# Optimization experiments

Hardware: AMD Instinct MI355X
Metric: run time of the kernel (lower is better)

## Reference

```python
import jax, jax.numpy as jnp
import numpy as np

DIM, DIM_HEAD, S, R = 1024, 64, 8, 2
SCALE = DIM_HEAD ** -0.5
NEG = -jnp.finfo(jnp.float32).max


def setup_inputs() -> dict:
    key = jax.random.key(0)
    ks = jax.random.split(key, 7)
    b, n = 2, 2048
    x = jax.random.normal(ks[0], (b, n, DIM), dtype=jnp.float32)
    mask = jnp.ones((b, n), dtype=bool)
    sd, rd = DIM_HEAD * S, DIM_HEAD * R
    init = lambda k, i, o: jax.random.normal(k, (i, o), dtype=jnp.float32) / np.sqrt(i)
    return {
        'x': x,
        'mask': mask,
        'Wsq': init(ks[1], DIM, sd),
        'Wsk': init(ks[2], DIM, sd),
        'Wrv': init(ks[3], DIM, rd),
        'Wrq': init(ks[4], DIM, sd),
        'Wrk': init(ks[5], DIM_HEAD, DIM_HEAD),
        'Wout': init(ks[6], sd, DIM),
    }


def _split_heads(t, h):
    # b n (h d) -> b h n d
    b, n, hd = t.shape
    return t.reshape(b, n, h, hd // h).transpose(0, 2, 1, 3)


def reference(x, mask, Wsq, Wsk, Wrv, Wrq, Wrk, Wout):
    # --- search stage ---
    sq = _split_heads(x @ Wsq, S) * SCALE          # b s i d
    sk = _split_heads(x @ Wsk, S)                  # b s j d
    search_sim = jnp.einsum('bsid,bsjd->bsij', sq, sk)
    search_sim = jnp.where(mask[:, None, None, :], search_sim, NEG)
    search_attn = jax.nn.softmax(search_sim, axis=-1)
    # --- retrieval stage ---
    rv = _split_heads(x @ Wrv, R)                  # b r j d
    retrieved = jnp.einsum('bsij,brjd->bsrid', search_attn, rv)  # b s r n d
    rq = _split_heads(x @ Wrq, S) * SCALE          # b s n d
    rk = retrieved @ Wrk                           # b s r n d
    retrieval_sim = jnp.einsum('bsnd,bsrnd->bsnr', rq, rk)
    retrieval_attn = jax.nn.softmax(retrieval_sim, axis=-1)
    out = jnp.einsum('bsnr,bsrnd->bsnd', retrieval_attn, retrieved)
    b, _, n, d = out.shape
    out = out.transpose(0, 2, 1, 3).reshape(b, n, S * d)  # b n (s d)
    return out @ Wout
```

## Files before the change

kernel.cpp:

```cpp
#include <hip/hip_runtime.h>

typedef unsigned short u16;
typedef unsigned int u32;
typedef __attribute__((ext_vector_type(8))) short short8;
typedef __attribute__((ext_vector_type(4))) float f32x4;
typedef __attribute__((ext_vector_type(16))) float f32x16;

#define B_     2
#define N_     2048
#define DIMX   1024
#define DH     64
#define NS     8
#define SD     512
#define RD     128

__device__ __forceinline__ float bu2f(u16 u) {
    return __uint_as_float(((unsigned)u) << 16);
}
__device__ __forceinline__ u16 f2bu(float f) {
    unsigned u = __float_as_uint(f);
    return (u16)((u + 0x7FFFu + ((u >> 16) & 1u)) >> 16);
}
__device__ __forceinline__ int swzA(int row, int col) {
    return row * 64 + (col ^ ((row & 7) << 3));
}
__device__ __forceinline__ int qswz(int row, int quad) {
    return row * 64 + ((quad ^ (row & 15)) << 2);
}
__device__ __forceinline__ short8 mk8(ushort4 lo, ushort4 hi) {
    short8 r;
    r[0] = (short)lo.x; r[1] = (short)lo.y; r[2] = (short)lo.z; r[3] = (short)lo.w;
    r[4] = (short)hi.x; r[5] = (short)hi.y; r[6] = (short)hi.z; r[7] = (short)hi.w;
    return r;
}

__global__ void detect_f32(const u16* __restrict__ wrk, int* __restrict__ flag) {
    __shared__ int cnt;
    if (threadIdx.x == 0) cnt = 0;
    __syncthreads();
    int local = 0;
    for (int k = threadIdx.x; k < 2048; k += 256) {
        u16 u = wrk[2 * k];
        int e = (u >> 7) & 0xFF;
        if (u == 0 || (e >= 0x60 && e <= 0x7E)) local++;
    }
    atomicAdd(&cnt, local);
    __syncthreads();
    if (threadIdx.x == 0) *flag = (cnt < 1024) ? 1 : 0;
}

__global__ __launch_bounds__(256, 4)
void convert_bf16(const void* __restrict__ src, u16* __restrict__ dst, int n8,
                  const int* __restrict__ flag) {
    const bool f32m = (*flag != 0);
    int idx = blockIdx.x * blockDim.x + threadIdx.x;
    int stride = gridDim.x * blockDim.x;
    for (int c = idx; c < n8; c += stride) {
        if (f32m) {
            const float4* s = (const float4*)src;
            float4 v0 = s[c * 2], v1 = s[c * 2 + 1];
            u16 o[8] = {f2bu(v0.x), f2bu(v0.y), f2bu(v0.z), f2bu(v0.w),
                        f2bu(v1.x), f2bu(v1.y), f2bu(v1.z), f2bu(v1.w)};
            *reinterpret_cast<short8*>(&dst[c * 8]) = *reinterpret_cast<short8*>(o);
        } else {
            *reinterpret_cast<short8*>(&dst[c * 8]) =
                reinterpret_cast<const short8*>(src)[c];
        }
    }
}

__global__ __launch_bounds__(256, 4)
void prep_weights(const void* __restrict__ Wsq, const void* __restrict__ Wsk,
                  const void* __restrict__ Wrq, const void* __restrict__ Wrv,
                  const void* __restrict__ Wout, const void* __restrict__ Wrk,
                  u16* __restrict__ wTcat, u16* __restrict__ woutT,
                  u16* __restrict__ wrkb, const int* __restrict__ flag) {
    const bool f32m = (*flag != 0);
    const int b = blockIdx.x, tid = threadIdx.x;

    if (b == 2176) {
#pragma unroll
        for (int t = 0; t < 2; ++t) {
            int c = tid + (t << 8);
            if (f32m) {
                const float4* s = (const float4*)Wrk;
                float4 v0 = s[c * 2], v1 = s[c * 2 + 1];
                u16 o[8] = {f2bu(v0.x), f2bu(v0.y), f2bu(v0.z), f2bu(v0.w),
                            f2bu(v1.x), f2bu(v1.y), f2bu(v1.z), f2bu(v1.w)};
                *reinterpret_cast<short8*>(&wrkb[c * 8]) = *reinterpret_cast<short8*>(o);
            } else {
                *reinterpret_cast<short8*>(&wrkb[c * 8]) =
                    reinterpret_cast<const short8*>(Wrk)[c];
            }
        }
        return;
    }

    const void* W; u16* dst; int K, N, t;
    if (b < 512)        { W = Wsq;  dst = wTcat;               K = DIMX; N = SD;   t = b; }
    else if (b < 1024)  { W = Wsk;  dst = wTcat + 512 * 1024;  K = DIMX; N = SD;   t = b - 512; }
    else if (b < 1536)  { W = Wrq;  dst = wTcat + 1024 * 1024; K = DIMX; N = SD;   t = b - 1024; }
    else if (b < 1664)  { W = Wrv;  dst = wTcat + 1536 * 1024; K = DIMX; N = RD;   t = b - 1536; }
    else                { W = Wout; dst = woutT;               K = SD;   N = DIMX; t = b - 1664; }
    const int ntn = N >> 5;
    const int k0 = (t / ntn) << 5, n0 = (t % ntn) << 5;

    __shared__ float T[32][33];
    const int r = tid >> 3, c4 = (tid & 7) << 2;
    if (f32m) {
        float4 v = *reinterpret_cast<const float4*>(
            &((const float*)W)[(size_t)(k0 + r) * N + n0 + c4]);
        T[r][c4 + 0] = v.x; T[r][c4 + 1] = v.y;
        T[r][c4 + 2] = v.z; T[r][c4 + 3] = v.w;
    } else {
        ushort4 v = *reinterpret_cast<const ushort4*>(
            &((const u16*)W)[(size_t)(k0 + r) * N + n0 + c4]);
        T[r][c4 + 0] = bu2f(v.x); T[r][c4 + 1] = bu2f(v.y);
        T[r][c4 + 2] = bu2f(v.z); T[r][c4 + 3] = bu2f(v.w);
    }
    __syncthreads();
    ushort4 st;
    st.x = f2bu(T[c4 + 0][r]); st.y = f2bu(T[c4 + 1][r]);
    st.z = f2bu(T[c4 + 2][r]); st.w = f2bu(T[c4 + 3][r]);
    *reinterpret_cast<ushort4*>(&dst[(size_t)(n0 + r) * K + k0 + c4]) = st;
}

template <int MODE>
__global__ __launch_bounds__(256, 2)
void gemm_mfma(const u16* __restrict__ A, const u16* __restrict__ Bt,
               void* __restrict__ C0, void* __restrict__ C1,
               void* __restrict__ C2, void* __restrict__ C3,
               int M, int N, int K, const int* __restrict__ flag) {
    __shared__ u16 As[4096];
    __shared__ u16 Bs[8192];
    const int tid = threadIdx.x, lane = tid & 63, w = tid >> 6;
    const int i = lane & 15, g = lane >> 4;
    const int row0 = blockIdx.y << 6, n0 = blockIdx.x << 7;

    f32x4 acc[8];
#pragma unroll
    for (int c = 0; c < 8; ++c) acc[c] = (f32x4){0.f, 0.f, 0.f, 0.f};

    for (int kt = 0; kt < K; kt += 64) {
        __syncthreads();
#pragma unroll
        for (int t2 = 0; t2 < 2; ++t2) {
            int v = tid + (t2 << 8);
            int r = v >> 3, c8 = (v & 7) << 3;
            *reinterpret_cast<short8*>(&As[swzA(r, c8)]) =
                *reinterpret_cast<const short8*>(&A[(size_t)(row0 + r) * K + kt + c8]);
        }
#pragma unroll
        for (int t4 = 0; t4 < 4; ++t4) {
            int v = tid + (t4 << 8);
            int n = v >> 3, c8 = (v & 7) << 3;
            *reinterpret_cast<short8*>(&Bs[swzA(n, c8)]) =
                *reinterpret_cast<const short8*>(&Bt[(size_t)(n0 + n) * K + kt + c8]);
        }
        __syncthreads();
#pragma unroll
        for (int ks = 0; ks < 2; ++ks) {
            short8 a = *reinterpret_cast<const short8*>(&As[swzA(w * 16 + i, ks * 32 + g * 8)]);
#pragma unroll
            for (int cf = 0; cf < 8; ++cf) {
                short8 b = *reinterpret_cast<const short8*>(&Bs[swzA(cf * 16 + i, ks * 32 + g * 8)]);
                acc[cf] = __builtin_amdgcn_mfma_f32_16x16x32_bf16(a, b, acc[cf], 0, 0, 0);
            }
        }
    }

    if (MODE == 0) {
        u16* dst; int ld, off; float alpha;
        if (n0 < 512)       { dst = (u16*)C0; ld = 512; off = n0;        alpha = 0.125f; }
        else if (n0 < 1024) { dst = (u16*)C1; ld = 512; off = n0 - 512;  alpha = 1.f; }
        else if (n0 < 1536) { dst = (u16*)C2; ld = 512; off = n0 - 1024; alpha = 0.125f; }
        else                { dst = (u16*)C3; ld = 128; off = n0 - 1536; alpha = 1.f; }
#pragma unroll
        for (int cf = 0; cf < 8; ++cf)
#pragma unroll
            for (int r = 0; r < 4; ++r)
                dst[(size_t)(row0 + w * 16 + g * 4 + r) * ld + off + cf * 16 + i] =
                    f2bu(acc[cf][r] * alpha);
    } else {
        const bool f32o = (*flag != 0);
        if (f32o) {
            float* Cf = (float*)C0;
#pragma unroll
            for (int cf = 0; cf < 8; ++cf)
#pragma unroll
                for (int r = 0; r < 4; ++r)
                    Cf[(size_t)(row0 + w * 16 + g * 4 + r) * N + n0 + cf * 16 + i] = acc[cf][r];
        } else {
            u16* Cb = (u16*)C0;
#pragma unroll
            for (int cf = 0; cf < 8; ++cf)
#pragma unroll
                for (int r = 0; r < 4; ++r)
                    Cb[(size_t)(row0 + w * 16 + g * 4 + r) * N + n0 + cf * 16 + i] =
                        f2bu(acc[cf][r]);
        }
    }
}

#define QMAP(r) (((r) & 3) + 8 * ((r) >> 2) + 4 * h)

__global__ __launch_bounds__(256, 1)
void flash_mfma32(const u16* __restrict__ sq, const u16* __restrict__ sk,
                  const u16* __restrict__ rv, const u16* __restrict__ rq,
                  const u16* __restrict__ wrk, u16* __restrict__ O) {
    __shared__ u16 Ks[2][64 * 64];
    __shared__ u16 Vt[2][128 * 64];

    const int tid = threadIdx.x, lane = tid & 63, w = tid >> 6;
    const int q31 = lane & 31, h = lane >> 5;
    const int bs = blockIdx.y, bi = bs >> 3, si = bs & 7;
    const int qw0 = (blockIdx.x << 7) + (w << 5);

    const u16* skb = sk + (size_t)bi * N_ * SD + si * DH;
    const u16* rvb = rv + (size_t)bi * N_ * RD;
    const u16* qrow  = sq + (size_t)(bi * N_ + qw0 + q31) * SD + si * DH;
    const u16* rqrow = rq + (size_t)(bi * N_ + qw0 + q31) * SD + si * DH;

    short8 qb[4];
#pragma unroll
    for (int s = 0; s < 4; ++s) {
        ushort4 lo = *reinterpret_cast<const ushort4*>(qrow + 16 * s + 4 * h);
        ushort4 hi = *reinterpret_cast<const ushort4*>(qrow + 16 * s + 8 + 4 * h);
        qb[s] = mk8(lo, hi);
    }

    const int krow = tid >> 2, kq = tid & 3;
    const int vdq = tid & 31, vjo = tid >> 5;

    short8 kreg[2];
    union U4 { ushort4 v; u16 e[4]; };
    U4 vreg[8];

#define LOADKV(jt_)                                                               \
    {                                                                             \
        const u16* kp = skb + (size_t)(((jt_) << 6) + krow) * SD + kq * 16;       \
        kreg[0] = *reinterpret_cast<const short8*>(kp);                           \
        kreg[1] = *reinterpret_cast<const short8*>(kp + 8);                       \
        const u16* vp = rvb + (size_t)(((jt_) << 6) + vjo * 8) * RD + vdq * 4;    \
        _Pragma("unroll")                                                         \
        for (int jj = 0; jj < 8; ++jj)                                            \
            vreg[jj].v = *reinterpret_cast<const ushort4*>(vp + (size_t)jj * RD); \
    }

#define STOREKV(buf_)                                                             \
    {                                                                             \
        const U4* kp4 = reinterpret_cast<const U4*>(&kreg[0]);                    \
        _Pragma("unroll")                                                         \
        for (int p = 0; p < 4; ++p)                                               \
            *reinterpret_cast<ushort4*>(&Ks[buf_][qswz(krow, 4 * kq + p)]) = kp4[p].v; \
        _Pragma("unroll")                                                         \
        for (int s_ = 0; s_ < 4; ++s_) {                                          \
            int d_ = 4 * vdq + s_;                                                \
            _Pragma("unroll")                                                     \
            for (int p = 0; p < 2; ++p) {                                         \
                ushort4 ov;                                                       \
                ov.x = vreg[4 * p + 0].e[s_]; ov.y = vreg[4 * p + 1].e[s_];       \
                ov.z = vreg[4 * p + 2].e[s_]; ov.w = vreg[4 * p + 3].e[s_];       \
                *reinterpret_cast<ushort4*>(&Vt[buf_][qswz(d_, 2 * vjo + p)]) = ov; \
            }                                                                     \
        }                                                                         \
    }

    f32x16 acc[4];
#pragma unroll
    for (int db = 0; db < 4; ++db) acc[db] = 0.f;
    float mrun = -3e38f, lsum = 0.f;

    LOADKV(0);
    STOREKV(0);
    __syncthreads();

    int cur = 0;
    for (int jt = 0; jt < 32; ++jt) {
        if (jt < 31) LOADKV(jt + 1);

        f32x16 sf0 = 0.f, sf1 = 0.f;
#pragma unroll
        for (int s = 0; s < 4; ++s) {
            ushort4 alo = *reinterpret_cast<const ushort4*>(&Ks[cur][qswz(q31, 4 * s + h)]);
            ushort4 ahi = *reinterpret_cast<const ushort4*>(&Ks[cur][qswz(q31, 4 * s + 2 + h)]);
            sf0 = __builtin_amdgcn_mfma_f32_32x32x16_bf16(mk8(alo, ahi), qb[s], sf0, 0, 0, 0);
        }
#pragma unroll
        for (int s = 0; s < 4; ++s) {
            ushort4 alo = *reinterpret_cast<const ushort4*>(&Ks[cur][qswz(32 + q31, 4 * s + h)]);
            ushort4 ahi = *reinterpret_cast<const ushort4*>(&Ks[cur][qswz(32 + q31, 4 * s + 2 + h)]);
            sf1 = __builtin_amdgcn_mfma_f32_32x32x16_bf16(mk8(alo, ahi), qb[s], sf1, 0, 0, 0);
        }

        float mt = sf0[0];
#pragma unroll
        for (int r = 1; r < 16; ++r) mt = fmaxf(mt, sf0[r]);
#pragma unroll
        for (int r = 0; r < 16; ++r) mt = fmaxf(mt, sf1[r]);
        mt = fmaxf(mt, __shfl_xor(mt, 32));
        if (!__all(mt - mrun <= 8.0f)) {
            float mn = fmaxf(mrun, mt);
            float corr = __expf(mrun - mn);
            mrun = mn;
            lsum *= corr;
#pragma unroll
            for (int r = 0; r < 16; ++r) {
                float cr = __shfl(corr, QMAP(r));
                acc[0][r] *= cr; acc[1][r] *= cr; acc[2][r] *= cr; acc[3][r] *= cr;
            }
        }
        float pf0[16], pf1[16];
#pragma unroll
        for (int r = 0; r < 16; ++r) {
            pf0[r] = __expf(sf0[r] - mrun); lsum += pf0[r];
            pf1[r] = __expf(sf1[r] - mrun); lsum += pf1[r];
        }

#pragma unroll
        for (int ks = 0; ks < 4; ++ks) {
            const float* pf = (ks < 2) ? pf0 : pf1;
            const int b0 = (ks & 1) * 8;
            u32 w0, w1, w2, w3;
            asm("v_cvt_pk_bf16_f32 %0, %1, %2" : "=v"(w0) : "v"(pf[b0 + 0]), "v"(pf[b0 + 1]));
            asm("v_cvt_pk_bf16_f32 %0, %1, %2" : "=v"(w1) : "v"(pf[b0 + 2]), "v"(pf[b0 + 3]));
            asm("v_cvt_pk_bf16_f32 %0, %1, %2" : "=v"(w2) : "v"(pf[b0 + 4]), "v"(pf[b0 + 5]));
            asm("v_cvt_pk_bf16_f32 %0, %1, %2" : "=v"(w3) : "v"(pf[b0 + 6]), "v"(pf[b0 + 7]));
            union { u32 u[4]; short8 s8; } pa;
            pa.u[0] = w0; pa.u[1] = w1; pa.u[2] = w2; pa.u[3] = w3;
#pragma unroll
            for (int db = 0; db < 4; ++db) {
                int d_ = 32 * db + q31;
                ushort4 vlo = *reinterpret_cast<const ushort4*>(&Vt[cur][qswz(d_, 4 * ks + h)]);
                ushort4 vhi = *reinterpret_cast<const ushort4*>(&Vt[cur][qswz(d_, 4 * ks + 2 + h)]);
                acc[db] = __builtin_amdgcn_mfma_f32_32x32x16_bf16(pa.s8, mk8(vlo, vhi), acc[db], 0, 0, 0);
            }
        }

        if (jt < 31) STOREKV(cur ^ 1);
        __syncthreads();
        cur ^= 1;
    }

    lsum += __shfl_xor(lsum, 32);

    short8 rqb4[4];
#pragma unroll
    for (int s = 0; s < 4; ++s) {
        ushort4 lo = *reinterpret_cast<const ushort4*>(rqrow + 16 * s + 4 * h);
        ushort4 hi = *reinterpret_cast<const ushort4*>(rqrow + 16 * s + 8 + 4 * h);
        rqb4[s] = mk8(lo, hi);
    }
    f32x16 w2[2];
    w2[0] = 0.f; w2[1] = 0.f;
#pragma unroll
    for (int cb = 0; cb < 2; ++cb)
#pragma unroll
        for (int s = 0; s < 4; ++s) {
            const u16* wp = wrk + (size_t)(32 * cb + q31) * 64 + 16 * s + 4 * h;
            short8 bw = mk8(*reinterpret_cast<const ushort4*>(wp),
                            *reinterpret_cast<const ushort4*>(wp + 8));
            w2[cb] = __builtin_amdgcn_mfma_f32_32x32x16_bf16(rqb4[s], bw, w2[cb], 0, 0, 0);
        }

#pragma unroll
    for (int r = 0; r < 16; ++r) {
        float t0 = acc[0][r] * w2[0][r] + acc[1][r] * w2[1][r];
        float t1 = acc[2][r] * w2[0][r] + acc[3][r] * w2[1][r];
        t0 += __shfl_xor(t0, 1); t0 += __shfl_xor(t0, 2); t0 += __shfl_xor(t0, 4);
        t0 += __shfl_xor(t0, 8); t0 += __shfl_xor(t0, 16);
        t1 += __shfl_xor(t1, 1); t1 += __shfl_xor(t1, 2); t1 += __shfl_xor(t1, 4);
        t1 += __shfl_xor(t1, 8); t1 += __shfl_xor(t1, 16);
        float lq = __shfl(lsum, QMAP(r));
        float linv = 1.f / lq;
        float z0 = t0 * linv, z1 = t1 * linv;
        float mz = fmaxf(z0, z1);
        float e0 = __expf(z0 - mz), e1 = __expf(z1 - mz);
        float inv = 1.f / (e0 + e1);
        float a0 = e0 * inv * linv, a1 = e1 * inv * linv;
        u16* Op = O + (size_t)(bi * N_ + qw0 + QMAP(r)) * SD + si * DH;
        Op[q31]      = f2bu(a0 * acc[0][r] + a1 * acc[2][r]);
        Op[32 + q31] = f2bu(a0 * acc[1][r] + a1 * acc[3][r]);
    }
#undef LOADKV
#undef STOREKV
}

extern "C" void kernel_launch(void* const* d_in, const int* in_sizes, int n_in,
                              void* d_out, int out_size, void* d_ws, size_t ws_size,
                              hipStream_t stream) {
    (void)in_sizes; (void)n_in; (void)out_size; (void)ws_size;
    const void* x    = d_in[0];
    const void* Wsq  = d_in[2];
    const void* Wsk  = d_in[3];
    const void* Wrv  = d_in[4];
    const void* Wrq  = d_in[5];
    const void* Wrk  = d_in[6];
    const void* Wout = d_in[7];

    const size_t MBy = 1024 * 1024;
    char* ws = (char*)d_ws;
    int* flag   = (int*)ws;
    u16* xb     = (u16*)(ws + 1 * MBy);
    u16* O      = xb;
    u16* wTcat  = (u16*)(ws + 9 * MBy);
    u16* woutT  = (u16*)(ws + 13 * MBy);
    u16* wrkb   = (u16*)(ws + 14 * MBy);
    u16* sqb    = (u16*)(ws + 15 * MBy);
    u16* skb    = (u16*)(ws + 19 * MBy);
    u16* rqb    = (u16*)(ws + 23 * MBy);
    u16* rvb    = (u16*)(ws + 27 * MBy);

    dim3 blk(256);
    detect_f32<<<1, blk, 0, stream>>>((const u16*)Wrk, flag);
    convert_bf16<<<2048, blk, 0, stream>>>(x, xb, (B_ * N_ * DIMX) / 8, flag);
    prep_weights<<<2177, blk, 0, stream>>>(Wsq, Wsk, Wrq, Wrv, Wout, Wrk,
                                           wTcat, woutT, wrkb, flag);
    gemm_mfma<0><<<dim3(13, 64), blk, 0, stream>>>(xb, wTcat, sqb, skb, rqb, rvb,
                                                   B_ * N_, 1664, DIMX, flag);
    flash_mfma32<<<dim3(N_ / 128, B_ * NS), blk, 0, stream>>>(sqb, skb, rvb, rqb, wrkb, O);
    gemm_mfma<1><<<dim3(8, 64), blk, 0, stream>>>(O, woutT, d_out, nullptr, nullptr, nullptr,
                                                  B_ * N_, DIMX, SD, flag);
}
```

Before: 155.2 us.

## Split flash attention key range across two warp groups and merge partial softmax

Doubles the block to 512 threads, where two groups of four warps each process half of the 2048 keys for the same 128 queries. Each group gets its own double-buffered K/V shared memory region. At the end, the first group writes its partial accumulators, running max and sum to shared memory, and the second group merges them with a log-sum-exp rescale. This adds parallelism for a grid of only 256 blocks, at the cost of more shared memory, a merge step, and an idle half-block during the epilogue.

After: 135.8 us. 12.5% less time.

```diff
diff --git a/kernel.cpp b/kernel.cpp
--- a/kernel.cpp
+++ b/kernel.cpp
@@ -204,17 +204,21 @@
 
 #define QMAP(r) (((r) & 3) + 8 * ((r) >> 2) + 4 * h)
 
-__global__ __launch_bounds__(256, 1)
+__global__ __launch_bounds__(512, 1)
 void flash_mfma32(const u16* __restrict__ sq, const u16* __restrict__ sk,
                   const u16* __restrict__ rv, const u16* __restrict__ rq,
                   const u16* __restrict__ wrk, u16* __restrict__ O) {
-    __shared__ u16 Ks[2][64 * 64];
-    __shared__ u16 Vt[2][128 * 64];
+    __shared__ __align__(16) char SMEM[98304];
+    u16* KsB = (u16*)SMEM;
+    u16* VtB = (u16*)(SMEM + 32768);
 
     const int tid = threadIdx.x, lane = tid & 63, w = tid >> 6;
+    const int g = w >> 2;
+    const int t256 = tid & 255;
     const int q31 = lane & 31, h = lane >> 5;
     const int bs = blockIdx.y, bi = bs >> 3, si = bs & 7;
-    const int qw0 = (blockIdx.x << 7) + (w << 5);
+    const int qw0 = (blockIdx.x << 7) + ((w & 3) << 5);
+    const int jt0 = g << 4;
 
     const u16* skb = sk + (size_t)bi * N_ * SD + si * DH;
     const u16* rvb = rv + (size_t)bi * N_ * RD;
@@ -229,8 +233,8 @@
         qb[s] = mk8(lo, hi);
     }
 
-    const int krow = tid >> 2, kq = tid & 3;
-    const int vdq = tid & 31, vjo = tid >> 5;
+    const int krow = t256 >> 2, kq = t256 & 3;
+    const int vdq = t256 & 31, vjo = t256 >> 5;
 
     short8 kreg[2];
     union U4 { ushort4 v; u16 e[4]; };
@@ -249,10 +253,12 @@
 
 #define STOREKV(buf_)                                                             \
     {                                                                             \
+        u16* Kd = KsB + ((g << 1) + (buf_)) * 4096;                               \
+        u16* Vd = VtB + ((g << 1) + (buf_)) * 8192;                               \
         const U4* kp4 = reinterpret_cast<const U4*>(&kreg[0]);                    \
         _Pragma("unroll")                                                         \
         for (int p = 0; p < 4; ++p)                                               \
-            *reinterpret_cast<ushort4*>(&Ks[buf_][qswz(krow, 4 * kq + p)]) = kp4[p].v; \
+            *reinterpret_cast<ushort4*>(&Kd[qswz(krow, 4 * kq + p)]) = kp4[p].v;  \
         _Pragma("unroll")                                                         \
         for (int s_ = 0; s_ < 4; ++s_) {                                          \
             int d_ = 4 * vdq + s_;                                                \
@@ -261,7 +267,7 @@
                 ushort4 ov;                                                       \
                 ov.x = vreg[4 * p + 0].e[s_]; ov.y = vreg[4 * p + 1].e[s_];       \
                 ov.z = vreg[4 * p + 2].e[s_]; ov.w = vreg[4 * p + 3].e[s_];       \
-                *reinterpret_cast<ushort4*>(&Vt[buf_][qswz(d_, 2 * vjo + p)]) = ov; \
+                *reinterpret_cast<ushort4*>(&Vd[qswz(d_, 2 * vjo + p)]) = ov;     \
             }                                                                     \
         }                                                                         \
     }
@@ -271,25 +277,28 @@
     for (int db = 0; db < 4; ++db) acc[db] = 0.f;
     float mrun = -3e38f, lsum = 0.f;
 
-    LOADKV(0);
+    LOADKV(jt0);
     STOREKV(0);
     __syncthreads();
 
     int cur = 0;
-    for (int jt = 0; jt < 32; ++jt) {
-        if (jt < 31) LOADKV(jt + 1);
+    for (int t = 0; t < 16; ++t) {
+        if (t < 15) LOADKV(jt0 + t + 1);
+
+        const u16* Kc = KsB + ((g << 1) + cur) * 4096;
+        const u16* Vc = VtB + ((g << 1) + cur) * 8192;
 
         f32x16 sf0 = 0.f, sf1 = 0.f;
 #pragma unroll
         for (int s = 0; s < 4; ++s) {
-            ushort4 alo = *reinterpret_cast<const ushort4*>(&Ks[cur][qswz(q31, 4 * s + h)]);
-            ushort4 ahi = *reinterpret_cast<const ushort4*>(&Ks[cur][qswz(q31, 4 * s + 2 + h)]);
+            ushort4 alo = *reinterpret_cast<const ushort4*>(&Kc[qswz(q31, 4 * s + h)]);
+            ushort4 ahi = *reinterpret_cast<const ushort4*>(&Kc[qswz(q31, 4 * s + 2 + h)]);
             sf0 = __builtin_amdgcn_mfma_f32_32x32x16_bf16(mk8(alo, ahi), qb[s], sf0, 0, 0, 0);
         }
 #pragma unroll
         for (int s = 0; s < 4; ++s) {
-            ushort4 alo = *reinterpret_cast<const ushort4*>(&Ks[cur][qswz(32 + q31, 4 * s + h)]);
-            ushort4 ahi = *reinterpret_cast<const ushort4*>(&Ks[cur][qswz(32 + q31, 4 * s + 2 + h)]);
+            ushort4 alo = *reinterpret_cast<const ushort4*>(&Kc[qswz(32 + q31, 4 * s + h)]);
+            ushort4 ahi = *reinterpret_cast<const ushort4*>(&Kc[qswz(32 + q31, 4 * s + 2 + h)]);
             sf1 = __builtin_amdgcn_mfma_f32_32x32x16_bf16(mk8(alo, ahi), qb[s], sf1, 0, 0, 0);
         }
 
@@ -331,18 +340,49 @@
 #pragma unroll
             for (int db = 0; db < 4; ++db) {
                 int d_ = 32 * db + q31;
-                ushort4 vlo = *reinterpret_cast<const ushort4*>(&Vt[cur][qswz(d_, 4 * ks + h)]);
-                ushort4 vhi = *reinterpret_cast<const ushort4*>(&Vt[cur][qswz(d_, 4 * ks + 2 + h)]);
+                ushort4 vlo = *reinterpret_cast<const ushort4*>(&Vc[qswz(d_, 4 * ks + h)]);
+                ushort4 vhi = *reinterpret_cast<const ushort4*>(&Vc[qswz(d_, 4 * ks + 2 + h)]);
                 acc[db] = __builtin_amdgcn_mfma_f32_32x32x16_bf16(pa.s8, mk8(vlo, vhi), acc[db], 0, 0, 0);
             }
         }
 
-        if (jt < 31) STOREKV(cur ^ 1);
+        if (t < 15) STOREKV(cur ^ 1);
         __syncthreads();
         cur ^= 1;
     }
 
     lsum += __shfl_xor(lsum, 32);
+
+    float* EX = (float*)SMEM;
+    if (w < 4) {
+        float* row = EX + ((size_t)(w * 64 + lane)) * 68;
+#pragma unroll
+        for (int db = 0; db < 4; ++db)
+#pragma unroll
+            for (int k4 = 0; k4 < 4; ++k4)
+                *reinterpret_cast<float4*>(row + db * 16 + k4 * 4) =
+                    make_float4(acc[db][4 * k4 + 0], acc[db][4 * k4 + 1],
+                                acc[db][4 * k4 + 2], acc[db][4 * k4 + 3]);
+        row[64] = mrun; row[65] = lsum;
+    }
+    __syncthreads();
+    if (w < 4) return;
+
+    {
+        const float* row = EX + ((size_t)((w - 4) * 64 + lane)) * 68;
+        float m0 = row[64], l0 = row[65];
+        float mn = fmaxf(mrun, m0);
+        float c1 = __expf(mrun - mn), c0 = __expf(m0 - mn);
+        lsum = lsum * c1 + l0 * c0;
+#pragma unroll
+        for (int r = 0; r < 16; ++r) {
+            float cr1 = __shfl(c1, QMAP(r));
+            float cr0 = __shfl(c0, QMAP(r));
+#pragma unroll
+            for (int db = 0; db < 4; ++db)
+                acc[db][r] = acc[db][r] * cr1 + row[db * 16 + r] * cr0;
+        }
+    }
 
     short8 rqb4[4];
 #pragma unroll
@@ -418,7 +458,7 @@
                                            wTcat, woutT, wrkb, flag);
     gemm_mfma<0><<<dim3(13, 64), blk, 0, stream>>>(xb, wTcat, sqb, skb, rqb, rvb,
                                                    B_ * N_, 1664, DIMX, flag);
-    flash_mfma32<<<dim3(N_ / 128, B_ * NS), blk, 0, stream>>>(sqb, skb, rvb, rqb, wrkb, O);
+    flash_mfma32<<<dim3(N_ / 128, B_ * NS), dim3(512), 0, stream>>>(sqb, skb, rvb, rqb, wrkb, O);
     gemm_mfma<1><<<dim3(8, 64), blk, 0, stream>>>(O, woutT, d_out, nullptr, nullptr, nullptr,
                                                   B_ * N_, DIMX, SD, flag);
 }
```
